# Kernel tuning notes

Hardware: AMD Instinct MI355X
Metric: run time of the kernel (lower is better)

Reference implementation:

```python
import jax, jax.numpy as jnp
import numpy as np

EPS = 1e-7  # K.epsilon()


def setup_inputs() -> dict:
    key = jax.random.key(0)
    k1, k2, k3 = jax.random.split(key, 3)
    B, T, D = 32, 2048, 1024
    one = jax.random.normal(k1, (B, D), dtype=jnp.float32)
    many = jax.random.normal(k2, (B, T, D), dtype=jnp.float32)
    W = jax.random.normal(k3, (D, D), dtype=jnp.float32) * (1.0 / np.sqrt(D))
    return {"one": one, "many": many, "W": W}


def reference(one, many, W):
    # logits = batch_dot(tanh(many @ W), one, axes=[2,1]) -> [B, T]
    proj = jnp.tanh(jnp.einsum('btd,de->bte', many, W))       # [B,T,D]
    logits = jnp.einsum('btd,bd->bt', proj, one)               # [B,T]
    # stable softmax with Keras epsilon in denominator
    ai = jnp.exp(logits - jnp.max(logits, axis=-1, keepdims=True))
    att_weights = ai / (jnp.sum(ai, axis=-1, keepdims=True) + EPS)  # [B,T]
    result = jnp.einsum('btd,bt->bd', many, att_weights)       # [B,D]
    return result, att_weights
```

## Files before the change

### kernel.cpp

```cpp
#include <hip/hip_runtime.h>
#include <hip/hip_bf16.h>

typedef _Float16 half8v __attribute__((ext_vector_type(8)));
typedef __fp16  fp16x2 __attribute__((ext_vector_type(2)));
typedef float floatx4 __attribute__((ext_vector_type(4)));

#define NB 32
#define NT 2048
#define ND 1024
#define NM (NB * NT)

#define GL16(g, l)                                                             \
    __builtin_amdgcn_global_load_lds(                                          \
        (const __attribute__((address_space(1))) void*)(g),                    \
        (__attribute__((address_space(3))) void*)(l), 16, 0, 0)

__device__ __forceinline__ float fast_tanh(float x) {
    x = fminf(9.0f, fmaxf(-9.0f, x));
    float e = __builtin_amdgcn_exp2f(x * 2.8853900817779268f);
    return (e - 1.0f) * __builtin_amdgcn_rcpf(e + 1.0f);
}

__global__ __launch_bounds__(256)
void zero_kernel(float* __restrict__ out, float* __restrict__ logits) {
    int i = blockIdx.x * 256 + threadIdx.x;
    logits[i] = 0.f;
    if (i < NB * ND) out[i] = 0.f;
}

__global__ __launch_bounds__(256)
void wt_kernel(const float* __restrict__ W, _Float16* __restrict__ Wt) {
    __shared__ float tile[32][33];
    int tx = threadIdx.x, ty = threadIdx.y;
    int bx = blockIdx.x, by = blockIdx.y;
    #pragma unroll
    for (int i = 0; i < 4; ++i) {
        int y = by * 32 + ty + i * 8;
        tile[ty + i * 8][tx] = W[y * ND + bx * 32 + tx];
    }
    __syncthreads();
    #pragma unroll
    for (int i = 0; i < 4; ++i) {
        int e = bx * 32 + ty + i * 8;
        Wt[e * ND + by * 32 + tx] = (_Float16)tile[tx][ty + i * 8];
    }
}

__global__ __launch_bounds__(256, 3)
void gemm_logits(const float* __restrict__ many, const _Float16* __restrict__ Wt,
                 const float* __restrict__ one, float* __restrict__ logits) {
    __shared__ uint4 AsQ[2048];
    __shared__ uint4 BsQ[1024];
    char* AsB = (char*)AsQ;
    char* BsB = (char*)BsQ;

    int bid = blockIdx.x;
    int j = (bid & 7) * 512 + (bid >> 3);
    int mb = j >> 3, nb = j & 7;
    int m0 = mb * 128, n0 = nb * 128;

    int tid = threadIdx.x;
    int lane = tid & 63, w = tid >> 6;
    int wr = w >> 1, wc = w & 1;
    int l15 = lane & 15, l4 = lane >> 4;

    const char* aS = (const char*)many + ((size_t)(m0 + (tid >> 4)) << 12)
        + (size_t)(((tid & 15) ^ ((tid >> 4) & 7)) << 4);
    const char* bS = (const char*)Wt + ((size_t)(n0 + (tid >> 3)) << 11)
        + (size_t)(((tid & 7) ^ ((tid >> 3) & 7)) << 4);
    char* aD = AsB + tid * 16;
    char* bD = BsB + tid * 16;

    floatx4 acc[4][4] = {};

    #pragma unroll 1
    for (int kb = 0; kb < 1024; kb += 64) {
        #pragma unroll
        for (int i = 0; i < 8; ++i)
            GL16(aS + kb * 4 + i * 65536, aD + i * 4096);
        #pragma unroll
        for (int i = 0; i < 4; ++i)
            GL16(bS + kb * 2 + i * 65536, bD + i * 4096);
        __syncthreads();

        #pragma unroll
        for (int ks = 0; ks < 64; ks += 32) {
            half8v af[4], bf[4];
            #pragma unroll
            for (int mi = 0; mi < 4; ++mi) {
                int r = wr * 64 + mi * 16 + l15;
                int s = l15 & 7;
                const char* base = AsB + r * 256;
                int c0 = (ks >> 2) + l4 * 2;
                float4 x = *(const float4*)(base + (size_t)((c0 ^ s) << 4));
                float4 y = *(const float4*)(base + (size_t)(((c0 + 1) ^ s) << 4));
                union { fp16x2 p[4]; half8v h; } u;
                u.p[0] = __builtin_amdgcn_cvt_pkrtz(x.x, x.y);
                u.p[1] = __builtin_amdgcn_cvt_pkrtz(x.z, x.w);
                u.p[2] = __builtin_amdgcn_cvt_pkrtz(y.x, y.y);
                u.p[3] = __builtin_amdgcn_cvt_pkrtz(y.z, y.w);
                af[mi] = u.h;
            }
            #pragma unroll
            for (int ni = 0; ni < 4; ++ni) {
                int r = wc * 64 + ni * 16 + l15;
                int s = l15 & 7;
                int c = (ks >> 3) + l4;
                bf[ni] = *(const half8v*)(BsB + r * 128 + (size_t)((c ^ s) << 4));
            }
            #pragma unroll
            for (int mi = 0; mi < 4; ++mi)
                #pragma unroll
                for (int ni = 0; ni < 4; ++ni)
                    acc[mi][ni] = __builtin_amdgcn_mfma_f32_16x16x32_f16(
                        af[mi], bf[ni], acc[mi][ni], 0, 0, 0);
        }
        __syncthreads();
    }

    int bidx = m0 >> 11;
    float onev[4];
    #pragma unroll
    for (int ni = 0; ni < 4; ++ni)
        onev[ni] = one[(bidx << 10) + n0 + wc * 64 + ni * 16 + l15];

    #pragma unroll
    for (int mi = 0; mi < 4; ++mi) {
        float part[4] = {0.f, 0.f, 0.f, 0.f};
        #pragma unroll
        for (int ni = 0; ni < 4; ++ni)
            #pragma unroll
            for (int b = 0; b < 4; ++b)
                part[b] += fast_tanh(acc[mi][ni][b]) * onev[ni];
        #pragma unroll
        for (int off = 1; off < 16; off <<= 1)
            #pragma unroll
            for (int b = 0; b < 4; ++b)
                part[b] += __shfl_xor(part[b], off, 64);
        #pragma unroll
        for (int b = 0; b < 4; ++b)
            if (l15 == mi * 4 + b)
                atomicAdd(&logits[m0 + wr * 64 + mi * 16 + l4 * 4 + b], part[b]);
    }
}

__global__ __launch_bounds__(256)
void softmax_kernel(const float* __restrict__ logits, float* __restrict__ att) {
    int b = blockIdx.x, tid = threadIdx.x;
    const float* lr = logits + (b << 11);
    float lv[8];
    float mx = -1e30f;
    #pragma unroll
    for (int i = 0; i < 8; ++i) { lv[i] = lr[tid + (i << 8)]; mx = fmaxf(mx, lv[i]); }
    #pragma unroll
    for (int off = 1; off < 64; off <<= 1) mx = fmaxf(mx, __shfl_xor(mx, off, 64));
    __shared__ float redm[4];
    __shared__ float reds[4];
    int wv = tid >> 6;
    if ((tid & 63) == 0) redm[wv] = mx;
    __syncthreads();
    mx = fmaxf(fmaxf(redm[0], redm[1]), fmaxf(redm[2], redm[3]));
    float s = 0.f;
    #pragma unroll
    for (int i = 0; i < 8; ++i) { lv[i] = expf(lv[i] - mx); s += lv[i]; }
    #pragma unroll
    for (int off = 1; off < 64; off <<= 1) s += __shfl_xor(s, off, 64);
    if ((tid & 63) == 0) reds[wv] = s;
    __syncthreads();
    s = reds[0] + reds[1] + reds[2] + reds[3];
    float inv = 1.0f / (s + 1e-7f);
    #pragma unroll
    for (int i = 0; i < 8; ++i) att[(b << 11) + tid + (i << 8)] = lv[i] * inv;
}

__global__ __launch_bounds__(256)
void out_kernel(const float* __restrict__ many, const float* __restrict__ att,
                float* __restrict__ out) {
    int b = blockIdx.x >> 4, tch = blockIdx.x & 15;
    int tid = threadIdx.x;
    __shared__ float aw[128];
    if (tid < 128) aw[tid] = att[(b << 11) + tch * 128 + tid];
    __syncthreads();
    const float* mp = many + (((size_t)b * NT + tch * 128) << 10) + tid * 4;
    float ax = 0.f, ay = 0.f, az = 0.f, aww = 0.f;
    for (int t = 0; t < 128; ++t) {
        float wgt = aw[t];
        float4 v = *reinterpret_cast<const float4*>(mp + ((size_t)t << 10));
        ax = fmaf(v.x, wgt, ax); ay = fmaf(v.y, wgt, ay);
        az = fmaf(v.z, wgt, az); aww = fmaf(v.w, wgt, aww);
    }
    float* op = out + (b << 10) + tid * 4;
    atomicAdd(op + 0, ax); atomicAdd(op + 1, ay);
    atomicAdd(op + 2, az); atomicAdd(op + 3, aww);
}

extern "C" void kernel_launch(void* const* d_in, const int* in_sizes, int n_in,
                              void* d_out, int out_size, void* d_ws, size_t ws_size,
                              hipStream_t stream) {
    const float* one  = (const float*)d_in[0];
    const float* many = (const float*)d_in[1];
    const float* W    = (const float*)d_in[2];
    float* out = (float*)d_out;

    _Float16* Wt     = (_Float16*)d_ws;
    float*    logits = (float*)((char*)d_ws + (size_t)ND * ND * 2);
    float*    att    = out + NB * ND;

    zero_kernel<<<256, 256, 0, stream>>>(out, logits);
    wt_kernel<<<dim3(32, 32), dim3(32, 8), 0, stream>>>(W, Wt);
    gemm_logits<<<4096, 256, 0, stream>>>(many, Wt, one, logits);
    softmax_kernel<<<NB, 256, 0, stream>>>(logits, att);
    out_kernel<<<NB * 16, 256, 0, stream>>>(many, att, out);
}
```

Measured before the change: 240.9 us.

## Halve GEMM LDS footprint by staging A tile in two half-K passes

The fp32 A tile is now loaded into shared memory in two 32-column halves per 64-wide K block instead of all at once, so the A buffer drops from 32KB to 16KB and total LDS per block falls from 48KB to 32KB. The launch bound is raised from 3 to 4 blocks per CU to use the freed LDS for higher occupancy. In exchange, each K iteration now has four barriers instead of two, and the second A load cannot start until the first half has been consumed, which adds serialization.

```diff
diff --git a/kernel.cpp b/kernel.cpp
--- a/kernel.cpp
+++ b/kernel.cpp
@@ -46,13 +46,11 @@
     }
 }
 
-__global__ __launch_bounds__(256, 3)
+__global__ __launch_bounds__(256, 4)
 void gemm_logits(const float* __restrict__ many, const _Float16* __restrict__ Wt,
                  const float* __restrict__ one, float* __restrict__ logits) {
-    __shared__ uint4 AsQ[2048];
-    __shared__ uint4 BsQ[1024];
-    char* AsB = (char*)AsQ;
-    char* BsB = (char*)BsQ;
+    __shared__ uint4 LDSQ[2048];
+    char* Ld = (char*)LDSQ;
 
     int bid = blockIdx.x;
     int j = (bid & 7) * 512 + (bid >> 3);
@@ -64,59 +62,62 @@
     int wr = w >> 1, wc = w & 1;
     int l15 = lane & 15, l4 = lane >> 4;
 
-    const char* aS = (const char*)many + ((size_t)(m0 + (tid >> 4)) << 12)
-        + (size_t)(((tid & 15) ^ ((tid >> 4) & 7)) << 4);
+    const char* aS = (const char*)many + ((size_t)(m0 + (tid >> 3)) << 12)
+        + (size_t)(((tid & 7) ^ ((tid >> 3) & 7)) << 4);
     const char* bS = (const char*)Wt + ((size_t)(n0 + (tid >> 3)) << 11)
         + (size_t)(((tid & 7) ^ ((tid >> 3) & 7)) << 4);
-    char* aD = AsB + tid * 16;
-    char* bD = BsB + tid * 16;
 
     floatx4 acc[4][4] = {};
+
+#define CHALF(H) do {                                                          \
+        half8v af[4], bf[4];                                                   \
+        _Pragma("unroll")                                                      \
+        for (int mi = 0; mi < 4; ++mi) {                                       \
+            int r = wr * 64 + mi * 16 + l15;                                   \
+            int s = r & 7;                                                     \
+            const char* base = Ld + r * 128;                                   \
+            float4 x = *(const float4*)(base + (((l4 * 2) ^ s) << 4));         \
+            float4 y = *(const float4*)(base + (((l4 * 2 + 1) ^ s) << 4));     \
+            union { fp16x2 p[4]; half8v h; } u;                                \
+            u.p[0] = __builtin_amdgcn_cvt_pkrtz(x.x, x.y);                     \
+            u.p[1] = __builtin_amdgcn_cvt_pkrtz(x.z, x.w);                     \
+            u.p[2] = __builtin_amdgcn_cvt_pkrtz(y.x, y.y);                     \
+            u.p[3] = __builtin_amdgcn_cvt_pkrtz(y.z, y.w);                     \
+            af[mi] = u.h;                                                      \
+        }                                                                      \
+        _Pragma("unroll")                                                      \
+        for (int ni = 0; ni < 4; ++ni) {                                       \
+            int r = wc * 64 + ni * 16 + l15;                                   \
+            int c = (H) * 4 + l4;                                              \
+            bf[ni] = *(const half8v*)(Ld + 16384 + r * 128 + ((c ^ (r & 7)) << 4)); \
+        }                                                                      \
+        _Pragma("unroll")                                                      \
+        for (int mi = 0; mi < 4; ++mi)                                         \
+            _Pragma("unroll")                                                  \
+            for (int ni = 0; ni < 4; ++ni)                                     \
+                acc[mi][ni] = __builtin_amdgcn_mfma_f32_16x16x32_f16(          \
+                    af[mi], bf[ni], acc[mi][ni], 0, 0, 0);                     \
+    } while (0)
 
     #pragma unroll 1
     for (int kb = 0; kb < 1024; kb += 64) {
         #pragma unroll
-        for (int i = 0; i < 8; ++i)
-            GL16(aS + kb * 4 + i * 65536, aD + i * 4096);
-        #pragma unroll
         for (int i = 0; i < 4; ++i)
-            GL16(bS + kb * 2 + i * 65536, bD + i * 4096);
-        __syncthreads();
-
-        #pragma unroll
-        for (int ks = 0; ks < 64; ks += 32) {
-            half8v af[4], bf[4];
-            #pragma unroll
-            for (int mi = 0; mi < 4; ++mi) {
-                int r = wr * 64 + mi * 16 + l15;
-                int s = l15 & 7;
-                const char* base = AsB + r * 256;
-                int c0 = (ks >> 2) + l4 * 2;
-                float4 x = *(const float4*)(base + (size_t)((c0 ^ s) << 4));
-                float4 y = *(const float4*)(base + (size_t)(((c0 + 1) ^ s) << 4));
-                union { fp16x2 p[4]; half8v h; } u;
-                u.p[0] = __builtin_amdgcn_cvt_pkrtz(x.x, x.y);
-                u.p[1] = __builtin_amdgcn_cvt_pkrtz(x.z, x.w);
-                u.p[2] = __builtin_amdgcn_cvt_pkrtz(y.x, y.y);
-                u.p[3] = __builtin_amdgcn_cvt_pkrtz(y.z, y.w);
-                af[mi] = u.h;
-            }
-            #pragma unroll
-            for (int ni = 0; ni < 4; ++ni) {
-                int r = wc * 64 + ni * 16 + l15;
-                int s = l15 & 7;
-                int c = (ks >> 3) + l4;
-                bf[ni] = *(const half8v*)(BsB + r * 128 + (size_t)((c ^ s) << 4));
-            }
-            #pragma unroll
-            for (int mi = 0; mi < 4; ++mi)
-                #pragma unroll
-                for (int ni = 0; ni < 4; ++ni)
-                    acc[mi][ni] = __builtin_amdgcn_mfma_f32_16x16x32_f16(
-                        af[mi], bf[ni], acc[mi][ni], 0, 0, 0);
-        }
-        __syncthreads();
-    }
+            GL16(bS + kb * 2 + i * 65536, Ld + 16384 + i * 4096 + tid * 16);
+        #pragma unroll
+        for (int i = 0; i < 4; ++i)
+            GL16(aS + kb * 4 + i * 131072, Ld + i * 4096 + tid * 16);
+        __syncthreads();
+        CHALF(0);
+        __syncthreads();
+        #pragma unroll
+        for (int i = 0; i < 4; ++i)
+            GL16(aS + kb * 4 + 128 + i * 131072, Ld + i * 4096 + tid * 16);
+        __syncthreads();
+        CHALF(1);
+        __syncthreads();
+    }
+#undef CHALF
 
     int bidx = m0 >> 11;
     float onev[4];
```

Result: no change. 241.0 us (+0.1%).
